# Kernel tuning notes

Hardware: AMD Instinct MI355X
Metric: run time of the kernel (lower is better)

Reference implementation:

```python
import jax, jax.numpy as jnp
import numpy as np

T = 4096
STATE_DIM = 400
EMBED_DIM = 300
WIDTH_DIM = 20
HID = 150
GI_DIM = 2 * STATE_DIM + EMBED_DIM + WIDTH_DIM
BINS = (1, 2, 3, 4, 8, 16, 32, 64)
MAX_W = 10


def _dtoi(d):
    return sum(1 for b in BINS if d >= b)


def _mlp(x, W1, b1, W2, b2, W3, b3):
    h = jax.nn.relu(x @ W1 + b1)
    h = jax.nn.relu(h @ W2 + b2)
    return h @ W3 + b3


def setup_inputs() -> dict:
    key = jax.random.key(0)
    ks = jax.random.split(key, 16)
    s = 0.02
    return {
        "embeds": jax.random.normal(ks[0], (T, EMBED_DIM), jnp.float32),
        "states": jax.random.normal(ks[1], (T, STATE_DIM), jnp.float32),
        # attention Scorer (state_dim -> 150 -> 150 -> 1)
        "aW1": jax.random.normal(ks[2], (STATE_DIM, HID), jnp.float32) * s,
        "ab1": jnp.zeros((HID,), jnp.float32),
        "aW2": jax.random.normal(ks[3], (HID, HID), jnp.float32) * s,
        "ab2": jnp.zeros((HID,), jnp.float32),
        "aW3": jax.random.normal(ks[4], (HID, 1), jnp.float32) * s,
        "ab3": jnp.zeros((1,), jnp.float32),
        # width embedding table: len(BINS)+1 rows
        "width_table": jax.random.normal(ks[5], (len(BINS) + 1, WIDTH_DIM), jnp.float32) * s,
        # sm Scorer (gi_dim -> 150 -> 150 -> 1)
        "sW1": jax.random.normal(ks[6], (GI_DIM, HID), jnp.float32) * s,
        "sb1": jnp.zeros((HID,), jnp.float32),
        "sW2": jax.random.normal(ks[7], (HID, HID), jnp.float32) * s,
        "sb2": jnp.zeros((HID,), jnp.float32),
        "sW3": jax.random.normal(ks[8], (HID, 1), jnp.float32) * s,
        "sb3": jnp.zeros((1,), jnp.float32),
    }


def reference(embeds, states, aW1, ab1, aW2, ab2, aW3, ab3, width_table,
              sW1, sb1, sW2, sb2, sW3, sb3):
    t = states.shape[0]
    attn_scores = _mlp(states, aW1, ab1, aW2, ab2, aW3, ab3)[:, 0]  # [T]

    gs_parts, width_parts = [], []
    for n in range(1, MAX_W + 1):  # fixed, small window-size loop
        w = t - n + 1
        starts = jnp.arange(w)
        idx = starts[:, None] + jnp.arange(n)[None, :]        # [W, n]
        a = jax.nn.softmax(attn_scores[idx], axis=1)           # per-span softmax
        pooled = jnp.einsum('wn,wnd->wd', a, embeds[idx])      # [W, embed]
        g = jnp.concatenate([states[starts], states[starts + n - 1], pooled], axis=1)
        gs_parts.append(g)
        width_parts.append(width_table[_dtoi(n)][None, :].repeat(w, axis=0))

    gs = jnp.concatenate(gs_parts, axis=0)                     # [S, 2*state+embed]
    widths = jnp.concatenate(width_parts, axis=0)              # [S, width_dim]
    gs = jnp.concatenate([gs, widths], axis=1)                 # [S, gi_dim]
    sms = _mlp(gs, sW1, sb1, sW2, sb2, sW3, sb3)[:, 0]         # [S]
    return sms
```

## Files before the change

kernel.cpp:

```cpp
#include <hip/hip_runtime.h>
#include <hip/hip_bf16.h>

#define T_TOK 4096
#define HID   150
#define HPAD  160
#define NSPAN 40915
#define MAXW  10
#define NT    10

typedef __attribute__((ext_vector_type(8))) _Float16 f16x8;
typedef __attribute__((ext_vector_type(4))) float    f32x4;

static __device__ __forceinline__ f16x8 cvt8(const float* __restrict__ row, int kbase, int K) {
    f16x8 a;
    if (kbase + 8 <= K) {
        float4 v0 = *(const float4*)(row + kbase);
        float4 v1 = *(const float4*)(row + kbase + 4);
        a[0] = (_Float16)v0.x; a[1] = (_Float16)v0.y;
        a[2] = (_Float16)v0.z; a[3] = (_Float16)v0.w;
        a[4] = (_Float16)v1.x; a[5] = (_Float16)v1.y;
        a[6] = (_Float16)v1.z; a[7] = (_Float16)v1.w;
    } else {
#pragma unroll
        for (int e = 0; e < 8; e++)
            a[e] = (_Float16)((kbase + e < K) ? row[kbase + e] : 0.f);
    }
    return a;
}

__global__ __launch_bounds__(256) void k_prep(
    const float* __restrict__ aW1, const float* __restrict__ sW1,
    const float* __restrict__ aW2, const float* __restrict__ sW2,
    const float* __restrict__ wt, const float* __restrict__ sb1,
    _Float16* __restrict__ fW1, _Float16* __restrict__ fA1,
    _Float16* __restrict__ fB1, _Float16* __restrict__ fE1,
    _Float16* __restrict__ fA2, _Float16* __restrict__ fW2,
    float* __restrict__ wc)
{
    const int b = blockIdx.x;
    const int w = threadIdx.x >> 6, l = threadIdx.x & 63;

    if (b < 148) {
        int tw = b * 4 + w;
        if (tw >= 590) return;
        const float* src; int srcK, off; _Float16* d;
        if      (tw < 130) { src = aW1;             srcK = 400; off = 0;   d = fW1; }
        else if (tw < 260) { src = sW1;             srcK = 400; off = 130; d = fA1; }
        else if (tw < 390) { src = sW1 + 400 * HID; srcK = 400; off = 260; d = fB1; }
        else if (tw < 490) { src = sW1 + 800 * HID; srcK = 300; off = 390; d = fE1; }
        else if (tw < 540) { src = aW2;             srcK = 150; off = 490; d = fA2; }
        else               { src = sW2;             srcK = 150; off = 540; d = fW2; }
        int tb = tw - off;
        int kt = tb / NT, nt = tb - kt * NT;
        int n = nt * 16 + (l & 15);
        int kbase = kt * 32 + (l >> 4) * 8;
        f16x8 hv;
#pragma unroll
        for (int e = 0; e < 8; e++) {
            int k = kbase + e;
            float f = (k < srcK && n < HID) ? src[(size_t)k * HID + n] : 0.f;
            hv[e] = (_Float16)f;
        }
        *(f16x8*)(d + ((size_t)tb * 64 + l) * 8) = hv;
    } else {
        int n = b - 147;
        int c = threadIdx.x;
        if (c >= HPAD) return;
        float s = 0.f;
        if (c < HID) {
            const int dt[11] = {0, 1, 2, 3, 4, 4, 4, 4, 5, 5, 5};
            const float* ww = wt + dt[n] * 20;
            s = sb1[c];
#pragma unroll
            for (int j = 0; j < 20; j++) s = fmaf(ww[j], sW1[(1100 + j) * HID + c], s);
        }
        wc[(n - 1) * HPAD + c] = s;
    }
}

__global__ __launch_bounds__(512) void k_proj(
    const float* __restrict__ states, const float* __restrict__ embeds,
    const _Float16* __restrict__ fW1, const _Float16* __restrict__ fA1,
    const _Float16* __restrict__ fB1, const _Float16* __restrict__ fE1,
    const _Float16* __restrict__ fA2,
    const float* __restrict__ ab1, const float* __restrict__ ab2,
    const float* __restrict__ aW3, const float* __restrict__ ab3,
    _Float16* __restrict__ Abuf, _Float16* __restrict__ Bbuf,
    _Float16* __restrict__ Ebuf, float* __restrict__ scores)
{
    __shared__ float smP[256 * 21];
    __shared__ alignas(16) _Float16 hh[5120];
    __shared__ float red[4][16];

    const float* Asrc; int lda, srcK, KT; const _Float16* Bf; _Float16* C = nullptr;
    switch (blockIdx.y) {
        case 0: Asrc = states; lda = 400; srcK = 400; KT = 13; Bf = fW1; break;
        case 1: Asrc = states; lda = 400; srcK = 400; KT = 13; Bf = fA1; C = Abuf; break;
        case 2: Asrc = states; lda = 400; srcK = 400; KT = 13; Bf = fB1; C = Bbuf; break;
        default:Asrc = embeds; lda = 300; srcK = 300; KT = 10; Bf = fE1; C = Ebuf; break;
    }
    const int tid = threadIdx.x;
    const int w   = tid >> 6, l = tid & 63;
    const int mtl = w >> 2;
    const int nh  = (w >> 1) & 1;
    const int kh  = w & 1;
    const int mt  = blockIdx.x * 2 + mtl;
    const int m15 = l & 15;
    const int koff = (l >> 4) * 8;
    const float* arow = Asrc + (size_t)(mt * 16 + m15) * lda;
    const f16x8* pB = (const f16x8*)Bf;
    const int pid = (mtl * 2 + nh) * 64 + l;

    f32x4 acc[5];
#pragma unroll
    for (int c = 0; c < 5; c++) acc[c] = (f32x4){0.f, 0.f, 0.f, 0.f};

    if (KT == 13) {
        if (kh == 0) {
#pragma unroll
            for (int kt = 0; kt < 7; ++kt) {
                f16x8 a = cvt8(arow, kt * 32 + koff, 400);
#pragma unroll
                for (int c = 0; c < 5; c++) {
                    f16x8 bv = pB[(size_t)(kt * NT + nh * 5 + c) * 64 + l];
                    acc[c] = __builtin_amdgcn_mfma_f32_16x16x32_f16(a, bv, acc[c], 0, 0, 0);
                }
            }
        } else {
#pragma unroll
            for (int kt = 7; kt < 13; ++kt) {
                f16x8 a = cvt8(arow, kt * 32 + koff, 400);
#pragma unroll
                for (int c = 0; c < 5; c++) {
                    f16x8 bv = pB[(size_t)(kt * NT + nh * 5 + c) * 64 + l];
                    acc[c] = __builtin_amdgcn_mfma_f32_16x16x32_f16(a, bv, acc[c], 0, 0, 0);
                }
            }
        }
    } else {
        if (kh == 0) {
#pragma unroll
            for (int kt = 0; kt < 5; ++kt) {
                f16x8 a = cvt8(arow, kt * 32 + koff, 300);
#pragma unroll
                for (int c = 0; c < 5; c++) {
                    f16x8 bv = pB[(size_t)(kt * NT + nh * 5 + c) * 64 + l];
                    acc[c] = __builtin_amdgcn_mfma_f32_16x16x32_f16(a, bv, acc[c], 0, 0, 0);
                }
            }
        } else {
#pragma unroll
            for (int kt = 5; kt < 10; ++kt) {
                f16x8 a = cvt8(arow, kt * 32 + koff, 300);
#pragma unroll
                for (int c = 0; c < 5; c++) {
                    f16x8 bv = pB[(size_t)(kt * NT + nh * 5 + c) * 64 + l];
                    acc[c] = __builtin_amdgcn_mfma_f32_16x16x32_f16(a, bv, acc[c], 0, 0, 0);
                }
            }
        }
    }

    if (kh == 1) {
#pragma unroll
        for (int c = 0; c < 5; c++)
#pragma unroll
            for (int r = 0; r < 4; r++) smP[pid * 21 + c * 4 + r] = acc[c][r];
    }
    __syncthreads();
    if (kh == 0) {
#pragma unroll
        for (int c = 0; c < 5; c++)
#pragma unroll
            for (int r = 0; r < 4; r++) acc[c][r] += smP[pid * 21 + c * 4 + r];
    }

    if (blockIdx.y != 0) {
        if (kh == 0) {
            const int m0 = mt * 16;
#pragma unroll
            for (int c = 0; c < 5; c++) {
                int col = (nh * 5 + c) * 16 + m15;
#pragma unroll
                for (int r = 0; r < 4; r++) {
                    int row = m0 + (l >> 4) * 4 + r;
                    C[(size_t)row * HPAD + col] = (_Float16)acc[c][r];
                }
            }
        }
        return;
    }

    if (kh == 0) {
#pragma unroll
        for (int c = 0; c < 5; c++) {
            int u   = nh * 5 + c;
            int col = u * 16 + m15;
            float bb = (col < HID) ? ab1[col] : 0.f;
            int kt2 = u >> 1;
            int g  = (u & 1) * 2 + (m15 >> 3);
            int e  = m15 & 7;
#pragma unroll
            for (int r = 0; r < 4; r++) {
                int rloc = (l >> 4) * 4 + r;
                float v = fmaxf(acc[c][r] + bb, 0.f);
                hh[((mtl * 5 + kt2) * 64 + g * 16 + rloc) * 8 + e] = (_Float16)v;
            }
        }
    }
    __syncthreads();

    if (kh == 0) {
        const f16x8* pH = (const f16x8*)hh;
        const f16x8* pB2 = (const f16x8*)fA2;
        f32x4 acc2[5];
#pragma unroll
        for (int c = 0; c < 5; c++) acc2[c] = (f32x4){0.f, 0.f, 0.f, 0.f};
#pragma unroll
        for (int kt = 0; kt < 5; ++kt) {
            f16x8 a = pH[(mtl * 5 + kt) * 64 + l];
#pragma unroll
            for (int c = 0; c < 5; c++) {
                f16x8 bv = pB2[(size_t)(kt * NT + nh * 5 + c) * 64 + l];
                acc2[c] = __builtin_amdgcn_mfma_f32_16x16x32_f16(a, bv, acc2[c], 0, 0, 0);
            }
        }
        float p[4] = {0.f, 0.f, 0.f, 0.f};
#pragma unroll
        for (int c = 0; c < 5; c++) {
            int col = (nh * 5 + c) * 16 + m15;
            float bb = (col < HID) ? ab2[col] : 0.f;
            float wv = (col < HID) ? aW3[col] : 0.f;
#pragma unroll
            for (int r = 0; r < 4; r++) {
                float v = fmaxf(acc2[c][r] + bb, 0.f);
                p[r] = fmaf(v, wv, p[r]);
            }
        }
#pragma unroll
        for (int off = 1; off < 16; off <<= 1)
#pragma unroll
            for (int r = 0; r < 4; r++) p[r] += __shfl_xor(p[r], off);
        if (m15 == 0)
#pragma unroll
            for (int r = 0; r < 4; r++) red[mtl * 2 + nh][(l >> 4) * 4 + r] = p[r];
    }
    __syncthreads();
    if (tid < 32) {
        scores[blockIdx.x * 32 + tid] =
            red[(tid >> 4) * 2 + 0][tid & 15] + red[(tid >> 4) * 2 + 1][tid & 15] + ab3[0];
    }
}

__global__ __launch_bounds__(256) void k_spanfinal(
    const float* __restrict__ scores, const _Float16* __restrict__ Abuf,
    const _Float16* __restrict__ Bbuf, const _Float16* __restrict__ Ebuf,
    const float* __restrict__ wc,
    const _Float16* __restrict__ fW2,
    const float* __restrict__ sb2, const float* __restrict__ sW3,
    const float* __restrict__ sb3, float* __restrict__ out)
{
    __shared__ alignas(16) _Float16 hh[5120];
    __shared__ float wg[32][10];
    __shared__ int   stI[32], nnI[32];
    __shared__ float red[4][16];

    const int tid = threadIdx.x;
    const int s0  = blockIdx.x * 32;

    {
        int sl = tid >> 3, k = tid & 7;
        int span = s0 + sl;
        int n = 1, start = 0;
        if (span < NSPAN) {
            int base = 0;
#pragma unroll
            for (int i = 1; i <= MAXW; i++) {
                int ww = T_TOK - i + 1;
                if (span < base + ww) { n = i; break; }
                base += ww;
            }
            start = span - base;
        }
        float x0 = (k < n)     ? scores[start + k]     : -1e30f;
        float x1 = (k + 8 < n) ? scores[start + k + 8] : -1e30f;
        float m = fmaxf(x0, x1);
        m = fmaxf(m, __shfl_xor(m, 1));
        m = fmaxf(m, __shfl_xor(m, 2));
        m = fmaxf(m, __shfl_xor(m, 4));
        float e0 = __expf(x0 - m), e1 = __expf(x1 - m);
        float s = e0 + e1;
        s += __shfl_xor(s, 1);
        s += __shfl_xor(s, 2);
        s += __shfl_xor(s, 4);
        float inv = 1.f / s;
        wg[sl][k] = e0 * inv;
        if (k < 2) wg[sl][k + 8] = e1 * inv;
        if (k == 0) { stI[sl] = start; nnI[sl] = n; }
    }
    __syncthreads();

#pragma unroll
    for (int it = 0; it < 3; ++it) {
        int task = it * 256 + tid;
        if (task < 640) {
            int sl = task / 20;
            int q  = task - sl * 20;
            int start = stI[sl];
            int nn = nnI[sl];
            int d0 = q * 8;
            f16x8 a8 = *(const f16x8*)(Abuf + (size_t)start * HPAD + d0);
            f16x8 b8 = *(const f16x8*)(Bbuf + (size_t)(start + nn - 1) * HPAD + d0);
            const float* wr = wc + (nn - 1) * HPAD + d0;
            float v[8];
#pragma unroll
            for (int e = 0; e < 8; e++) v[e] = (float)a8[e] + (float)b8[e] + wr[e];
#pragma unroll
            for (int i = 0; i < MAXW; i++) {
                int ridx = min(start + i, T_TOK - 1);
                f16x8 e8 = *(const f16x8*)(Ebuf + (size_t)ridx * HPAD + d0);
                float aa = wg[sl][i];
#pragma unroll
                for (int e = 0; e < 8; e++) v[e] = fmaf(aa, (float)e8[e], v[e]);
            }
            f16x8 hv;
#pragma unroll
            for (int e = 0; e < 8; e++) hv[e] = (_Float16)fmaxf(v[e], 0.f);
            int mtl = sl >> 4, smr = sl & 15;
            int kt = q >> 2, gg = q & 3;
            *(f16x8*)(hh + ((mtl * 5 + kt) * 64 + gg * 16 + smr) * 8) = hv;
        }
    }
    __syncthreads();

    const int w = tid >> 6, l = tid & 63;
    const int mtl = w >> 1, nh = w & 1;
    const int m15 = l & 15;
    const f16x8* pH = (const f16x8*)hh;
    const f16x8* pB = (const f16x8*)fW2;
    f32x4 acc[5];
#pragma unroll
    for (int c = 0; c < 5; c++) acc[c] = (f32x4){0.f, 0.f, 0.f, 0.f};
#pragma unroll
    for (int kt = 0; kt < 5; ++kt) {
        f16x8 a = pH[(mtl * 5 + kt) * 64 + l];
#pragma unroll
        for (int c = 0; c < 5; c++) {
            f16x8 bv = pB[(size_t)(kt * NT + nh * 5 + c) * 64 + l];
            acc[c] = __builtin_amdgcn_mfma_f32_16x16x32_f16(a, bv, acc[c], 0, 0, 0);
        }
    }
    float p[4] = {0.f, 0.f, 0.f, 0.f};
#pragma unroll
    for (int c = 0; c < 5; c++) {
        int col = (nh * 5 + c) * 16 + m15;
        float bb = (col < HID) ? sb2[col] : 0.f;
        float wv = (col < HID) ? sW3[col] : 0.f;
#pragma unroll
        for (int r = 0; r < 4; r++) {
            float v = fmaxf(acc[c][r] + bb, 0.f);
            p[r] = fmaf(v, wv, p[r]);
        }
    }
#pragma unroll
    for (int off = 1; off < 16; off <<= 1)
#pragma unroll
        for (int r = 0; r < 4; r++) p[r] += __shfl_xor(p[r], off);
    if (m15 == 0)
#pragma unroll
        for (int r = 0; r < 4; r++) red[w][(l >> 4) * 4 + r] = p[r];
    __syncthreads();
    if (tid < 32) {
        int row = s0 + tid;
        if (row < NSPAN)
            out[row] = red[(tid >> 4) * 2 + 0][tid & 15] +
                       red[(tid >> 4) * 2 + 1][tid & 15] + sb3[0];
    }
}

extern "C" void kernel_launch(void* const* d_in, const int* in_sizes, int n_in,
                              void* d_out, int out_size, void* d_ws, size_t ws_size,
                              hipStream_t stream) {
    const float* embeds = (const float*)d_in[0];
    const float* states = (const float*)d_in[1];
    const float* aW1 = (const float*)d_in[2];
    const float* ab1 = (const float*)d_in[3];
    const float* aW2 = (const float*)d_in[4];
    const float* ab2 = (const float*)d_in[5];
    const float* aW3 = (const float*)d_in[6];
    const float* ab3 = (const float*)d_in[7];
    const float* wt  = (const float*)d_in[8];
    const float* sW1 = (const float*)d_in[9];
    const float* sb1 = (const float*)d_in[10];
    const float* sW2 = (const float*)d_in[11];
    const float* sb2 = (const float*)d_in[12];
    const float* sW3 = (const float*)d_in[13];
    const float* sb3 = (const float*)d_in[14];
    float* out = (float*)d_out;

    char* W = (char*)d_ws;
    _Float16* Abuf = (_Float16*)(W + 0);
    _Float16* Bbuf = (_Float16*)(W + 1310720);
    _Float16* Ebuf = (_Float16*)(W + 2621440);
    float* scores  = (float*)(W + 3932160);
    float* wcbuf   = (float*)(W + 3948544);
    _Float16* fW1  = (_Float16*)(W + 3954944);
    _Float16* fA1  = (_Float16*)(W + 4088064);
    _Float16* fB1  = (_Float16*)(W + 4221184);
    _Float16* fE1  = (_Float16*)(W + 4354304);
    _Float16* fA2  = (_Float16*)(W + 4456704);
    _Float16* fW2  = (_Float16*)(W + 4507904);

    k_prep<<<158, 256, 0, stream>>>(aW1, sW1, aW2, sW2, wt, sb1,
                                    fW1, fA1, fB1, fE1, fA2, fW2, wcbuf);
    k_proj<<<dim3(128, 4), 512, 0, stream>>>(states, embeds,
        fW1, fA1, fB1, fE1, fA2, ab1, ab2, aW3, ab3, Abuf, Bbuf, Ebuf, scores);
    k_spanfinal<<<1279, 256, 0, stream>>>(scores, Abuf, Bbuf, Ebuf, wcbuf,
        fW2, sb2, sW3, sb3, out);
}
```

Measured before the change: 37.60 us.

## Reuse states fragments across three projections and stage span rows in LDS

k_proj now loads and converts each block's states rows to fp16 registers once and reuses them for the A, B and attention-W1 projections, with embeds handled by a separate grid row. This halves the grid from four to two y-slices. k_spanfinal copies the contiguous window of A/B/E rows covering its 32 spans into shared memory, so the gather loop reads LDS instead of re-reading global rows. The change adds register pressure, shared memory use and extra barriers, which may lower occupancy, and it serializes three GEMMs in one block.

```diff
diff --git a/kernel.cpp b/kernel.cpp
--- a/kernel.cpp
+++ b/kernel.cpp
@@ -92,13 +92,6 @@
     __shared__ alignas(16) _Float16 hh[5120];
     __shared__ float red[4][16];
 
-    const float* Asrc; int lda, srcK, KT; const _Float16* Bf; _Float16* C = nullptr;
-    switch (blockIdx.y) {
-        case 0: Asrc = states; lda = 400; srcK = 400; KT = 13; Bf = fW1; break;
-        case 1: Asrc = states; lda = 400; srcK = 400; KT = 13; Bf = fA1; C = Abuf; break;
-        case 2: Asrc = states; lda = 400; srcK = 400; KT = 13; Bf = fB1; C = Bbuf; break;
-        default:Asrc = embeds; lda = 300; srcK = 300; KT = 10; Bf = fE1; C = Ebuf; break;
-    }
     const int tid = threadIdx.x;
     const int w   = tid >> 6, l = tid & 63;
     const int mtl = w >> 2;
@@ -107,75 +100,33 @@
     const int mt  = blockIdx.x * 2 + mtl;
     const int m15 = l & 15;
     const int koff = (l >> 4) * 8;
-    const float* arow = Asrc + (size_t)(mt * 16 + m15) * lda;
-    const f16x8* pB = (const f16x8*)Bf;
     const int pid = (mtl * 2 + nh) * 64 + l;
 
-    f32x4 acc[5];
-#pragma unroll
-    for (int c = 0; c < 5; c++) acc[c] = (f32x4){0.f, 0.f, 0.f, 0.f};
-
-    if (KT == 13) {
-        if (kh == 0) {
-#pragma unroll
-            for (int kt = 0; kt < 7; ++kt) {
-                f16x8 a = cvt8(arow, kt * 32 + koff, 400);
-#pragma unroll
-                for (int c = 0; c < 5; c++) {
-                    f16x8 bv = pB[(size_t)(kt * NT + nh * 5 + c) * 64 + l];
-                    acc[c] = __builtin_amdgcn_mfma_f32_16x16x32_f16(a, bv, acc[c], 0, 0, 0);
-                }
-            }
-        } else {
-#pragma unroll
-            for (int kt = 7; kt < 13; ++kt) {
-                f16x8 a = cvt8(arow, kt * 32 + koff, 400);
-#pragma unroll
-                for (int c = 0; c < 5; c++) {
-                    f16x8 bv = pB[(size_t)(kt * NT + nh * 5 + c) * 64 + l];
-                    acc[c] = __builtin_amdgcn_mfma_f32_16x16x32_f16(a, bv, acc[c], 0, 0, 0);
-                }
-            }
-        }
-    } else {
-        if (kh == 0) {
-#pragma unroll
-            for (int kt = 0; kt < 5; ++kt) {
-                f16x8 a = cvt8(arow, kt * 32 + koff, 300);
-#pragma unroll
-                for (int c = 0; c < 5; c++) {
-                    f16x8 bv = pB[(size_t)(kt * NT + nh * 5 + c) * 64 + l];
-                    acc[c] = __builtin_amdgcn_mfma_f32_16x16x32_f16(a, bv, acc[c], 0, 0, 0);
-                }
-            }
-        } else {
-#pragma unroll
-            for (int kt = 5; kt < 10; ++kt) {
-                f16x8 a = cvt8(arow, kt * 32 + koff, 300);
-#pragma unroll
-                for (int c = 0; c < 5; c++) {
-                    f16x8 bv = pB[(size_t)(kt * NT + nh * 5 + c) * 64 + l];
-                    acc[c] = __builtin_amdgcn_mfma_f32_16x16x32_f16(a, bv, acc[c], 0, 0, 0);
-                }
-            }
-        }
-    }
-
-    if (kh == 1) {
-#pragma unroll
-        for (int c = 0; c < 5; c++)
-#pragma unroll
-            for (int r = 0; r < 4; r++) smP[pid * 21 + c * 4 + r] = acc[c][r];
-    }
-    __syncthreads();
-    if (kh == 0) {
-#pragma unroll
-        for (int c = 0; c < 5; c++)
-#pragma unroll
-            for (int r = 0; r < 4; r++) acc[c][r] += smP[pid * 21 + c * 4 + r];
-    }
-
-    if (blockIdx.y != 0) {
+    if (blockIdx.y == 1) {
+        const float* arow = embeds + (size_t)(mt * 16 + m15) * 300;
+        f16x8 afr[5];
+#pragma unroll
+        for (int i = 0; i < 5; i++) afr[i] = cvt8(arow, (kh * 5 + i) * 32 + koff, 300);
+        f32x4 acc[5];
+#pragma unroll
+        for (int c = 0; c < 5; c++) acc[c] = (f32x4){0.f, 0.f, 0.f, 0.f};
+        const f16x8* pB = (const f16x8*)fE1;
+#pragma unroll
+        for (int i = 0; i < 5; i++) {
+            int ktg = kh * 5 + i;
+#pragma unroll
+            for (int c = 0; c < 5; c++) {
+                f16x8 bv = pB[(size_t)(ktg * NT + nh * 5 + c) * 64 + l];
+                acc[c] = __builtin_amdgcn_mfma_f32_16x16x32_f16(afr[i], bv, acc[c], 0, 0, 0);
+            }
+        }
+        if (kh == 1) {
+#pragma unroll
+            for (int c = 0; c < 5; c++)
+#pragma unroll
+                for (int r = 0; r < 4; r++) smP[pid * 21 + c * 4 + r] = acc[c][r];
+        }
+        __syncthreads();
         if (kh == 0) {
             const int m0 = mt * 16;
 #pragma unroll
@@ -184,31 +135,92 @@
 #pragma unroll
                 for (int r = 0; r < 4; r++) {
                     int row = m0 + (l >> 4) * 4 + r;
-                    C[(size_t)row * HPAD + col] = (_Float16)acc[c][r];
+                    Ebuf[(size_t)row * HPAD + col] =
+                        (_Float16)(acc[c][r] + smP[pid * 21 + c * 4 + r]);
                 }
             }
         }
         return;
     }
 
+    const float* arow = states + (size_t)(mt * 16 + m15) * 400;
+    f16x8 afr[7];
     if (kh == 0) {
 #pragma unroll
-        for (int c = 0; c < 5; c++) {
-            int u   = nh * 5 + c;
-            int col = u * 16 + m15;
-            float bb = (col < HID) ? ab1[col] : 0.f;
-            int kt2 = u >> 1;
-            int g  = (u & 1) * 2 + (m15 >> 3);
-            int e  = m15 & 7;
-#pragma unroll
-            for (int r = 0; r < 4; r++) {
-                int rloc = (l >> 4) * 4 + r;
-                float v = fmaxf(acc[c][r] + bb, 0.f);
-                hh[((mtl * 5 + kt2) * 64 + g * 16 + rloc) * 8 + e] = (_Float16)v;
-            }
-        }
-    }
-    __syncthreads();
+        for (int i = 0; i < 7; i++) afr[i] = cvt8(arow, i * 32 + koff, 400);
+    } else {
+#pragma unroll
+        for (int i = 0; i < 6; i++) afr[i] = cvt8(arow, (7 + i) * 32 + koff, 400);
+    }
+
+    for (int g = 0; g < 3; ++g) {
+        const f16x8* pB = (const f16x8*)(g == 0 ? fA1 : (g == 1 ? fB1 : fW1));
+        f32x4 acc[5];
+#pragma unroll
+        for (int c = 0; c < 5; c++) acc[c] = (f32x4){0.f, 0.f, 0.f, 0.f};
+        if (kh == 0) {
+#pragma unroll
+            for (int i = 0; i < 7; i++) {
+#pragma unroll
+                for (int c = 0; c < 5; c++) {
+                    f16x8 bv = pB[(size_t)(i * NT + nh * 5 + c) * 64 + l];
+                    acc[c] = __builtin_amdgcn_mfma_f32_16x16x32_f16(afr[i], bv, acc[c], 0, 0, 0);
+                }
+            }
+        } else {
+#pragma unroll
+            for (int i = 0; i < 6; i++) {
+#pragma unroll
+                for (int c = 0; c < 5; c++) {
+                    f16x8 bv = pB[(size_t)((7 + i) * NT + nh * 5 + c) * 64 + l];
+                    acc[c] = __builtin_amdgcn_mfma_f32_16x16x32_f16(afr[i], bv, acc[c], 0, 0, 0);
+                }
+            }
+        }
+        if (kh == 1) {
+#pragma unroll
+            for (int c = 0; c < 5; c++)
+#pragma unroll
+                for (int r = 0; r < 4; r++) smP[pid * 21 + c * 4 + r] = acc[c][r];
+        }
+        __syncthreads();
+        if (kh == 0) {
+#pragma unroll
+            for (int c = 0; c < 5; c++)
+#pragma unroll
+                for (int r = 0; r < 4; r++) acc[c][r] += smP[pid * 21 + c * 4 + r];
+            if (g < 2) {
+                _Float16* C = (g == 0) ? Abuf : Bbuf;
+                const int m0 = mt * 16;
+#pragma unroll
+                for (int c = 0; c < 5; c++) {
+                    int col = (nh * 5 + c) * 16 + m15;
+#pragma unroll
+                    for (int r = 0; r < 4; r++) {
+                        int row = m0 + (l >> 4) * 4 + r;
+                        C[(size_t)row * HPAD + col] = (_Float16)acc[c][r];
+                    }
+                }
+            } else {
+#pragma unroll
+                for (int c = 0; c < 5; c++) {
+                    int u   = nh * 5 + c;
+                    int col = u * 16 + m15;
+                    float bb = (col < HID) ? ab1[col] : 0.f;
+                    int kt2 = u >> 1;
+                    int gg  = (u & 1) * 2 + (m15 >> 3);
+                    int e   = m15 & 7;
+#pragma unroll
+                    for (int r = 0; r < 4; r++) {
+                        int rloc = (l >> 4) * 4 + r;
+                        float v = fmaxf(acc[c][r] + bb, 0.f);
+                        hh[((mtl * 5 + kt2) * 64 + gg * 16 + rloc) * 8 + e] = (_Float16)v;
+                    }
+                }
+            }
+        }
+        __syncthreads();
+    }
 
     if (kh == 0) {
         const f16x8* pH = (const f16x8*)hh;
@@ -261,8 +273,12 @@
     const float* __restrict__ sb3, float* __restrict__ out)
 {
     __shared__ alignas(16) _Float16 hh[5120];
+    __shared__ alignas(16) _Float16 Atile[32 * HPAD];
+    __shared__ alignas(16) _Float16 Btile[41 * HPAD];
+    __shared__ alignas(16) _Float16 Etile[41 * HPAD];
     __shared__ float wg[32][10];
     __shared__ int   stI[32], nnI[32];
+    __shared__ int   mm[2];
     __shared__ float red[4][16];
 
     const int tid = threadIdx.x;
@@ -300,6 +316,39 @@
     }
     __syncthreads();
 
+    if (tid == 0) {
+        int lo = stI[0], hi = stI[0] + nnI[0];
+#pragma unroll
+        for (int i = 1; i < 32; i++) {
+            lo = min(lo, stI[i]);
+            hi = max(hi, stI[i] + nnI[i]);
+        }
+        mm[0] = lo; mm[1] = hi;
+    }
+    __syncthreads();
+    const int m0 = mm[0];
+    const bool staged = (mm[1] - m0) <= 41;
+
+    if (staged) {
+        for (int t = tid; t < 2280; t += 256) {
+            int seg, row, q;
+            if (t < 640)       { seg = 0; row = t / 20;          q = t - row * 20; }
+            else if (t < 1460) { seg = 1; row = (t - 640) / 20;  q = (t - 640) - row * 20; }
+            else               { seg = 2; row = (t - 1460) / 20; q = (t - 1460) - row * 20; }
+            int gr = min(m0 + row, T_TOK - 1);
+            if (seg == 0)
+                *(f16x8*)(Atile + row * HPAD + q * 8) =
+                    *(const f16x8*)(Abuf + (size_t)gr * HPAD + q * 8);
+            else if (seg == 1)
+                *(f16x8*)(Btile + row * HPAD + q * 8) =
+                    *(const f16x8*)(Bbuf + (size_t)gr * HPAD + q * 8);
+            else
+                *(f16x8*)(Etile + row * HPAD + q * 8) =
+                    *(const f16x8*)(Ebuf + (size_t)gr * HPAD + q * 8);
+        }
+    }
+    __syncthreads();
+
 #pragma unroll
     for (int it = 0; it < 3; ++it) {
         int task = it * 256 + tid;
@@ -309,19 +358,35 @@
             int start = stI[sl];
             int nn = nnI[sl];
             int d0 = q * 8;
-            f16x8 a8 = *(const f16x8*)(Abuf + (size_t)start * HPAD + d0);
-            f16x8 b8 = *(const f16x8*)(Bbuf + (size_t)(start + nn - 1) * HPAD + d0);
-            const float* wr = wc + (nn - 1) * HPAD + d0;
             float v[8];
-#pragma unroll
-            for (int e = 0; e < 8; e++) v[e] = (float)a8[e] + (float)b8[e] + wr[e];
-#pragma unroll
-            for (int i = 0; i < MAXW; i++) {
-                int ridx = min(start + i, T_TOK - 1);
-                f16x8 e8 = *(const f16x8*)(Ebuf + (size_t)ridx * HPAD + d0);
-                float aa = wg[sl][i];
-#pragma unroll
-                for (int e = 0; e < 8; e++) v[e] = fmaf(aa, (float)e8[e], v[e]);
+            if (staged) {
+                f16x8 a8 = *(const f16x8*)(Atile + (start - m0) * HPAD + d0);
+                f16x8 b8 = *(const f16x8*)(Btile + (start + nn - 1 - m0) * HPAD + d0);
+                const float* wr = wc + (nn - 1) * HPAD + d0;
+#pragma unroll
+                for (int e = 0; e < 8; e++) v[e] = (float)a8[e] + (float)b8[e] + wr[e];
+#pragma unroll
+                for (int i = 0; i < MAXW; i++) {
+                    int rr = min(start + i - m0, 40);
+                    f16x8 e8 = *(const f16x8*)(Etile + rr * HPAD + d0);
+                    float aa = wg[sl][i];
+#pragma unroll
+                    for (int e = 0; e < 8; e++) v[e] = fmaf(aa, (float)e8[e], v[e]);
+                }
+            } else {
+                f16x8 a8 = *(const f16x8*)(Abuf + (size_t)start * HPAD + d0);
+                f16x8 b8 = *(const f16x8*)(Bbuf + (size_t)(start + nn - 1) * HPAD + d0);
+                const float* wr = wc + (nn - 1) * HPAD + d0;
+#pragma unroll
+                for (int e = 0; e < 8; e++) v[e] = (float)a8[e] + (float)b8[e] + wr[e];
+#pragma unroll
+                for (int i = 0; i < MAXW; i++) {
+                    int ridx = min(start + i, T_TOK - 1);
+                    f16x8 e8 = *(const f16x8*)(Ebuf + (size_t)ridx * HPAD + d0);
+                    float aa = wg[sl][i];
+#pragma unroll
+                    for (int e = 0; e < 8; e++) v[e] = fmaf(aa, (float)e8[e], v[e]);
+                }
             }
             f16x8 hv;
 #pragma unroll
@@ -413,7 +478,7 @@
 
     k_prep<<<158, 256, 0, stream>>>(aW1, sW1, aW2, sW2, wt, sb1,
                                     fW1, fA1, fB1, fE1, fA2, fW2, wcbuf);
-    k_proj<<<dim3(128, 4), 512, 0, stream>>>(states, embeds,
+    k_proj<<<dim3(128, 2), 512, 0, stream>>>(states, embeds,
         fW1, fA1, fB1, fE1, fA2, ab1, ab2, aW3, ab3, Abuf, Bbuf, Ebuf, scores);
     k_spanfinal<<<1279, 256, 0, stream>>>(scores, Abuf, Bbuf, Ebuf, wcbuf,
         fW2, sb2, sW3, sb3, out);
```

Measured after the change: 59.88 us. 1.59x slower.
